# Optimization experiments

Hardware: AMD Instinct MI355X
Metric: run time of the kernel (lower is better)

## Reference

```python
import jax, jax.numpy as jnp
import numpy as np

NUM_KERNELS = 50
KERNEL_DIM = 5


def setup_inputs() -> dict:
    key = jax.random.key(0)
    k1, k2 = jax.random.split(key)
    B, F = 1024, 512
    x = jax.random.normal(k1, (B, F), dtype=jnp.float32)
    # glorot-uniform-ish scale for T
    fan_in, fan_out = F, NUM_KERNELS * KERNEL_DIM
    limit = float(np.sqrt(6.0 / (fan_in + fan_out)))
    T = jax.random.uniform(k2, (F, fan_out), dtype=jnp.float32, minval=-limit, maxval=limit)
    return {"x": x, "T": T}


def reference(x, T):
    B = x.shape[0]
    # M: [B, K, D]
    M = (x @ T).reshape(B, NUM_KERNELS, KERNEL_DIM)
    # pairwise diffs: [B, K, D, B]  (M[i,k,d] - M[j,k,d])
    diffs = M[:, :, :, None] - jnp.transpose(M, (1, 2, 0))[None, :, :, :]
    abs_diffs = jnp.sum(jnp.abs(diffs), axis=2)          # [B, K, B]
    minibatch_features = jnp.sum(jnp.exp(-abs_diffs), axis=2)  # [B, K]
    return jnp.concatenate([x, minibatch_features], axis=1)
```

## Files before the change

kernel.cpp:

```cpp
#include <hip/hip_runtime.h>

#define B_SZ 1024
#define F_SZ 512
#define NK   50
#define KD   5
#define C_SZ 250
#define OUTW 562
#define PLANE (C_SZ * B_SZ)
#define NT   16
#define TILE 64
#define NPAIRS 136
#define PBLK  34
#define PART_ELEMS (NK * NT * B_SZ)
#define LOG2E 1.44269504088896340736f

__global__ __launch_bounds__(256) void gemm_copy_kernel(const float* __restrict__ x,
                                                        const float* __restrict__ T,
                                                        float* __restrict__ ws2,
                                                        float* __restrict__ out,
                                                        int zero_feat) {
    const int t = threadIdx.x;

    if (blockIdx.x >= 256) {
        const int b = blockIdx.x - 256;
#pragma unroll
        for (int r = 0; r < 8; ++r) {
            const int row = b * 8 + r;
            const float2* src = (const float2*)(x + (size_t)row * F_SZ);
            float2* dst = (float2*)(out + (size_t)row * OUTW);
            dst[t] = src[t];
            if (zero_feat && t < NK) out[(size_t)row * OUTW + F_SZ + t] = 0.0f;
        }
        return;
    }

    const int rt = blockIdx.x & 127;
    const int ks = blockIdx.x >> 7;
    if (t >= C_SZ) return;
    const int r0 = rt * 8;
    const int f0 = ks * 256;

    float acc[8] = {0.f, 0.f, 0.f, 0.f, 0.f, 0.f, 0.f, 0.f};
    const float* xp = x + (size_t)r0 * F_SZ + f0;
    const float* Tp = T + (size_t)f0 * C_SZ + t;

#pragma unroll 8
    for (int f = 0; f < 256; ++f) {
        const float tv = Tp[(size_t)f * C_SZ];
#pragma unroll
        for (int r = 0; r < 8; ++r)
            acc[r] += xp[r * F_SZ + f] * tv;
    }

    float* dst = ws2 + ((size_t)(ks * C_SZ + t)) * B_SZ + r0;
    float4 lo = make_float4(acc[0] * LOG2E, acc[1] * LOG2E,
                            acc[2] * LOG2E, acc[3] * LOG2E);
    float4 hi = make_float4(acc[4] * LOG2E, acc[5] * LOG2E,
                            acc[6] * LOG2E, acc[7] * LOG2E);
    ((float4*)dst)[0] = lo;
    ((float4*)dst)[1] = hi;
}

__device__ __forceinline__ float wave_ror1(float v) {
    return __int_as_float(__builtin_amdgcn_update_dpp(
        0, __float_as_int(v), 0x13C, 0xf, 0xf, false));
}

template <bool ATOMIC>
__global__ __launch_bounds__(256) void pair_kernel(const float* __restrict__ ws2,
                                                   float* __restrict__ part,
                                                   float* __restrict__ out) {
    const int bid  = blockIdx.x;
    const int k    = bid / PBLK;
    const int wv   = __builtin_amdgcn_readfirstlane(threadIdx.x >> 6);
    const int lane = threadIdx.x & 63;

    int p = (bid - k * PBLK) * 4 + wv;
    int ti = 0;
    while (p >= NT - ti) { p -= NT - ti; ++ti; }
    const int tj = ti + p;
    const int bi = ti * TILE;
    const int bj = tj * TILE;
    const bool diag = (ti == tj);

    const float* pa = ws2 + (size_t)k * (KD * B_SZ);
    const float* pb = pa + (size_t)PLANE;

    float mi[KD], mj[KD];
#pragma unroll
    for (int d = 0; d < KD; ++d) {
        mi[d] = pa[d * B_SZ + bi + lane] + pb[d * B_SZ + bi + lane];
        mj[d] = pa[d * B_SZ + bj + lane] + pb[d * B_SZ + bj + lane];
    }

    float acci = 0.0f;
    float vcol = 0.0f;

#pragma unroll 16
    for (int s = 0; s < TILE; ++s) {
        const float sum = __builtin_fabsf(mi[0] - mj[0])
                        + __builtin_fabsf(mi[1] - mj[1])
                        + __builtin_fabsf(mi[2] - mj[2])
                        + __builtin_fabsf(mi[3] - mj[3])
                        + __builtin_fabsf(mi[4] - mj[4]);
        const float e = __builtin_amdgcn_exp2f(-sum);
        acci += e;
        vcol += e;
        mj[0] = wave_ror1(mj[0]);
        mj[1] = wave_ror1(mj[1]);
        mj[2] = wave_ror1(mj[2]);
        mj[3] = wave_ror1(mj[3]);
        mj[4] = wave_ror1(mj[4]);
        vcol  = wave_ror1(vcol);
    }

    if (ATOMIC) {
        atomicAdd(&out[(size_t)(bi + lane) * OUTW + F_SZ + k], acci);
        if (!diag)
            atomicAdd(&out[(size_t)(bj + lane) * OUTW + F_SZ + k], vcol);
    } else {
        part[(size_t)(k * NT + tj) * B_SZ + bi + lane] = acci;
        if (!diag)
            part[(size_t)(k * NT + ti) * B_SZ + bj + lane] = vcol;
    }
}

__global__ __launch_bounds__(256) void reduce_kernel(const float* __restrict__ part,
                                                     float* __restrict__ out) {
    const int k = blockIdx.x >> 2;
    const int i = ((blockIdx.x & 3) << 8) | threadIdx.x;
    float s = 0.0f;
#pragma unroll
    for (int sp = 0; sp < NT; ++sp)
        s += part[((size_t)(k * NT + sp)) * B_SZ + i];
    out[(size_t)i * OUTW + F_SZ + k] = s;
}

extern "C" void kernel_launch(void* const* d_in, const int* in_sizes, int n_in,
                              void* d_out, int out_size, void* d_ws, size_t ws_size,
                              hipStream_t stream) {
    const float* x = (const float*)d_in[0];
    const float* T = (const float*)d_in[1];
    float* out = (float*)d_out;
    float* ws2 = (float*)d_ws;
    float* part = ws2 + 2 * (size_t)PLANE;

    const size_t need = (size_t)(2 * PLANE + PART_ELEMS) * 4;
    const int fast = (ws_size >= need);

    gemm_copy_kernel<<<384, 256, 0, stream>>>(x, T, ws2, out, fast ? 0 : 1);

    if (fast) {
        pair_kernel<false><<<NK * PBLK, 256, 0, stream>>>(ws2, part, out);
        reduce_kernel<<<200, 256, 0, stream>>>(part, out);
    } else {
        pair_kernel<true><<<NK * PBLK, 256, 0, stream>>>(ws2, nullptr, out);
    }
}
```

Measured before the change: 42.02 us.

## Register-block pair kernel as 4x16 per-lane tile instead of DPP rotation

Replaces the per-step DPP wave rotation of column values with a register-blocked scheme: each lane holds 4 row points and streams 16 column points loaded as float4 from global memory, accumulating row and column partial sums in registers. Row sums are reduced with cross-lane shuffles and column sums through a padded shared-memory transpose. This removes six DPP moves per pair evaluation and lets operands be reused across a 4x4 micro-tile. In exchange it raises register pressure, adds a shared-memory reduction, and issues redundant global loads of column data across lanes.

```diff
diff --git a/kernel.cpp b/kernel.cpp
--- a/kernel.cpp
+++ b/kernel.cpp
@@ -61,67 +61,92 @@
     ((float4*)dst)[1] = hi;
 }
 
-__device__ __forceinline__ float wave_ror1(float v) {
-    return __int_as_float(__builtin_amdgcn_update_dpp(
-        0, __float_as_int(v), 0x13C, 0xf, 0xf, false));
-}
-
 template <bool ATOMIC>
 __global__ __launch_bounds__(256) void pair_kernel(const float* __restrict__ ws2,
                                                    float* __restrict__ part,
                                                    float* __restrict__ out) {
+    __shared__ float colw[4][TILE][17];
+
     const int bid  = blockIdx.x;
     const int k    = bid / PBLK;
     const int wv   = __builtin_amdgcn_readfirstlane(threadIdx.x >> 6);
     const int lane = threadIdx.x & 63;
+    const int jg   = lane >> 4;
+    const int il   = lane & 15;
 
     int p = (bid - k * PBLK) * 4 + wv;
     int ti = 0;
     while (p >= NT - ti) { p -= NT - ti; ++ti; }
     const int tj = ti + p;
-    const int bi = ti * TILE;
-    const int bj = tj * TILE;
+    const int bi = ti * TILE, bj = tj * TILE;
     const bool diag = (ti == tj);
 
     const float* pa = ws2 + (size_t)k * (KD * B_SZ);
     const float* pb = pa + (size_t)PLANE;
 
-    float mi[KD], mj[KD];
+    float mi[4][KD];
 #pragma unroll
     for (int d = 0; d < KD; ++d) {
-        mi[d] = pa[d * B_SZ + bi + lane] + pb[d * B_SZ + bi + lane];
-        mj[d] = pa[d * B_SZ + bj + lane] + pb[d * B_SZ + bj + lane];
+        const float4 a = *(const float4*)(pa + d * B_SZ + bi + il * 4);
+        const float4 b = *(const float4*)(pb + d * B_SZ + bi + il * 4);
+        mi[0][d] = a.x + b.x; mi[1][d] = a.y + b.y;
+        mi[2][d] = a.z + b.z; mi[3][d] = a.w + b.w;
     }
 
-    float acci = 0.0f;
-    float vcol = 0.0f;
+    float acci[4] = {0.f, 0.f, 0.f, 0.f};
+    float colacc[16];
+#pragma unroll
+    for (int q = 0; q < 16; ++q) colacc[q] = 0.0f;
 
-#pragma unroll 16
-    for (int s = 0; s < TILE; ++s) {
-        const float sum = __builtin_fabsf(mi[0] - mj[0])
-                        + __builtin_fabsf(mi[1] - mj[1])
-                        + __builtin_fabsf(mi[2] - mj[2])
-                        + __builtin_fabsf(mi[3] - mj[3])
-                        + __builtin_fabsf(mi[4] - mj[4]);
-        const float e = __builtin_amdgcn_exp2f(-sum);
-        acci += e;
-        vcol += e;
-        mj[0] = wave_ror1(mj[0]);
-        mj[1] = wave_ror1(mj[1]);
-        mj[2] = wave_ror1(mj[2]);
-        mj[3] = wave_ror1(mj[3]);
-        mj[4] = wave_ror1(mj[4]);
-        vcol  = wave_ror1(vcol);
+#pragma unroll
+    for (int c4 = 0; c4 < 4; ++c4) {
+        const int jb = bj + jg * 16 + c4 * 4;
+        float4 cj[KD];
+#pragma unroll
+        for (int d = 0; d < KD; ++d) {
+            const float4 a = *(const float4*)(pa + d * B_SZ + jb);
+            const float4 b = *(const float4*)(pb + d * B_SZ + jb);
+            cj[d] = make_float4(a.x + b.x, a.y + b.y, a.z + b.z, a.w + b.w);
+        }
+#define PAIR_JJ(C, JJ)                                                           \
+        {                                                                        \
+            _Pragma("unroll")                                                    \
+            for (int r = 0; r < 4; ++r) {                                        \
+                const float s = __builtin_fabsf(mi[r][0] - cj[0].C)              \
+                              + __builtin_fabsf(mi[r][1] - cj[1].C)              \
+                              + __builtin_fabsf(mi[r][2] - cj[2].C)              \
+                              + __builtin_fabsf(mi[r][3] - cj[3].C)              \
+                              + __builtin_fabsf(mi[r][4] - cj[4].C);             \
+                const float e = __builtin_amdgcn_exp2f(-s);                      \
+                acci[r] += e;                                                    \
+                colacc[c4 * 4 + JJ] += e;                                        \
+            }                                                                    \
+        }
+        PAIR_JJ(x, 0) PAIR_JJ(y, 1) PAIR_JJ(z, 2) PAIR_JJ(w, 3)
+#undef PAIR_JJ
     }
 
-    if (ATOMIC) {
-        atomicAdd(&out[(size_t)(bi + lane) * OUTW + F_SZ + k], acci);
-        if (!diag)
-            atomicAdd(&out[(size_t)(bj + lane) * OUTW + F_SZ + k], vcol);
-    } else {
-        part[(size_t)(k * NT + tj) * B_SZ + bi + lane] = acci;
-        if (!diag)
-            part[(size_t)(k * NT + ti) * B_SZ + bj + lane] = vcol;
+#pragma unroll
+    for (int r = 0; r < 4; ++r) {
+        acci[r] += __shfl_xor(acci[r], 16, 64);
+        acci[r] += __shfl_xor(acci[r], 32, 64);
+    }
+    const float rsum = (jg == 0) ? acci[0] : (jg == 1) ? acci[1]
+                     : (jg == 2) ? acci[2] : acci[3];
+    const int rrow = bi + il * 4 + jg;
+    if (ATOMIC) atomicAdd(&out[(size_t)rrow * OUTW + F_SZ + k], rsum);
+    else        part[(size_t)(k * NT + tj) * B_SZ + rrow] = rsum;
+
+    if (!diag) {
+#pragma unroll
+        for (int q = 0; q < 16; ++q)
+            colw[wv][jg * 16 + q][il] = colacc[q];
+        float csum = 0.0f;
+#pragma unroll
+        for (int i2 = 0; i2 < 16; ++i2)
+            csum += colw[wv][lane][i2];
+        if (ATOMIC) atomicAdd(&out[(size_t)(bj + lane) * OUTW + F_SZ + k], csum);
+        else        part[(size_t)(k * NT + ti) * B_SZ + bj + lane] = csum;
     }
 }
 
```

After: 40.80 us. -2.9%, faster.
